# Kernel optimization log

Measured on AMD Instinct MI355X. Metric: run time of the kernel, lower is better.

## Reference

```python
import jax, jax.numpy as jnp
import numpy as np

FOCAL = 525.0
CX, CY = 320.0, 240.0
W_PROJ = 0.33   # loss_dict / energy_weights['proj']
W_BONE = 0.5    # loss_dict / energy_weights['bone']
B = 1_000_000
J = 21          # NUM_OF_JOINTS for 'mpi' model
NB = J - 1      # number of bone connections


def setup_inputs() -> dict:
    key = jax.random.key(0)
    k1, k2, k3 = jax.random.split(key, 3)
    # Poses: random joints shifted +10 in z so they sit in front of the camera
    # (avoids perspective divide by ~0).
    pose = jax.random.normal(k1, (B, 3, J), dtype=jnp.float32)
    pose = pose.at[:, 2, :].add(10.0)
    projected_est = jax.random.normal(k2, (B, 2, J), dtype=jnp.float32)
    bone_lengths = jax.random.uniform(k3, (NB,), dtype=jnp.float32) + 0.1
    R_drone = jnp.eye(3, dtype=jnp.float32)            # drone orientation
    C_drone = jnp.zeros((3, 1), dtype=jnp.float32)     # drone position
    # kinematic chain over 21 joints -> 20 bones
    bone_connections = jnp.stack(
        [jnp.arange(NB, dtype=jnp.int64), jnp.arange(1, J, dtype=jnp.int64)], axis=1)
    return {
        "future_pose3d": pose,
        "projected_est": projected_est,
        "bone_lengths": bone_lengths,
        "R_drone": R_drone,
        "C_drone": C_drone,
        "bone_connections": bone_connections,
    }


def _project(pose, R, C):
    # take_bone_projection: 2D = K @ R^T (P - C), then perspective divide.
    # pose: [B,3,J]
    K = jnp.array([[FOCAL, 0.0, CX], [0.0, FOCAL, CY], [0.0, 0.0, 1.0]],
                  dtype=pose.dtype)
    M = K @ R.T                                   # [3,3]
    proj = jnp.einsum('kc,bcj->bkj', M, pose - C[None, :, :])  # [B,3,J]
    return proj[:, :2, :] / proj[:, 2:3, :]      # [B,2,J]


def reference(future_pose3d, projected_est, bone_lengths, R_drone, C_drone,
              bone_connections):
    # --- projection MSE (per-sample mse_loss, averaged over batch) ---
    p2d = _project(future_pose3d, R_drone, C_drone)           # [B,2,J]
    n_el = 2.0 * J
    proj_loss = jnp.mean(jnp.sum((p2d - projected_est) ** 2, axis=(1, 2)) / n_el)

    # --- bone-length loss: gathered squared bone lengths vs targets ---
    d = (future_pose3d[:, :, bone_connections[:, 0]]
         - future_pose3d[:, :, bone_connections[:, 1]])        # [B,3,NB]
    sq_len = jnp.sum(d ** 2, axis=1)                           # [B,NB]
    bone_loss = jnp.mean(jnp.sum((bone_lengths[None, :] - sq_len) ** 2, axis=1)
                         / (J - 1))

    return W_PROJ * proj_loss + W_BONE * bone_loss
```

## Files before the change

### kernel.cpp

```cpp
#include <hip/hip_runtime.h>


namespace {

constexpr float F_    = 525.0f;
constexpr float CX_   = 320.0f;
constexpr float CY_   = 240.0f;
constexpr float WPROJ = 0.33f / 42.0f;
constexpr float WBONE = 0.5f  / 20.0f;
constexpr int   NT    = 64;
constexpr int   TILE  = 64;
constexpr int   PF4   = TILE * 63 / 4;
constexpr int   EF4   = TILE * 42 / 4;
constexpr int   TF4   = PF4 + EF4;
constexpr int   RFULL = TF4 / NT;
constexpr int   REM   = TF4 - RFULL*NT;
constexpr int   DMA_N = RFULL + 1;
constexpr int   NBLK  = 768;

constexpr int wcnt(int vm, int lgkm) {
    return (vm & 0xF) | ((vm >> 4) << 14) | (0x7 << 4) | ((lgkm & 0xF) << 8);
}

__device__ __forceinline__ long lmin(long a, long b) { return a < b ? a : b; }

__global__ __launch_bounds__(NT)
void pose_loss_kernel(const float* __restrict__ pose,
                      const float* __restrict__ est,
                      const float* __restrict__ bl,
                      const float* __restrict__ Rm,
                      const float* __restrict__ Cd,
                      float* __restrict__ out,
                      int B)
{
    __shared__ float4 smem[2 * TF4];

    const int tid = threadIdx.x;
    const float4* pose4 = (const float4*)pose;
    const float4* est4  = (const float4*)est;
    const long pmax = (long)B * 63 / 4 - 1;
    const long emax = (long)B * 42 / 4 - 1;
    const int  ntiles = (B + TILE - 1) / TILE;

    const float r0 = Rm[0], r1 = Rm[1], r2 = Rm[2];
    const float r3 = Rm[3], r4 = Rm[4], r5 = Rm[5];
    const float r6 = Rm[6], r7 = Rm[7], r8 = Rm[8];
    const float m00 = F_ * r0 + CX_ * r2;
    const float m01 = F_ * r3 + CX_ * r5;
    const float m02 = F_ * r6 + CX_ * r8;
    const float m10 = F_ * r1 + CY_ * r2;
    const float m11 = F_ * r4 + CY_ * r5;
    const float m12 = F_ * r7 + CY_ * r8;
    const float m20 = r2, m21 = r5, m22 = r8;
    const float c0 = Cd[0], c1 = Cd[1], c2 = Cd[2];
    float blv[20];
    #pragma unroll
    for (int i = 0; i < 20; ++i) blv[i] = bl[i];

    auto dma = [&](long T, int buf) {
        const long pb = T * PF4;
        const long eb = T * EF4 - PF4;
        float4* dst = &smem[buf * TF4];
        #pragma unroll
        for (int r = 0; r < RFULL; ++r) {
            const int f = r * NT + tid;
            const float4* g = (f < PF4) ? (pose4 + lmin(pb + f, pmax))
                                        : (est4  + lmin(eb + f, emax));
            __builtin_amdgcn_global_load_lds(
                (const __attribute__((address_space(1))) void*)g,
                (__attribute__((address_space(3))) void*)(dst + r * NT),
                16, 0, 0);
        }
        if (tid < REM) {
            const long gi = lmin(eb + RFULL * NT + tid, emax);
            __builtin_amdgcn_global_load_lds(
                (const __attribute__((address_space(1))) void*)(est4 + gi),
                (__attribute__((address_space(3))) void*)(&smem[buf*TF4 + RFULL*NT]),
                16, 0, 0);
        }
    };

    float accP = 0.0f, accB = 0.0f;
    long T = blockIdx.x;
    if (T < ntiles) dma(T, 0);

    int i = 0;
    while (T < ntiles) {
        const long Tn = T + NBLK;
        __asm__ __volatile__("" ::: "memory");
        __builtin_amdgcn_s_waitcnt(wcnt(63, 0));
        if (Tn < ntiles) {
            dma(Tn, (i + 1) & 1);
            __builtin_amdgcn_s_waitcnt(wcnt(DMA_N, 15));
        } else {
            __builtin_amdgcn_s_waitcnt(wcnt(0, 15));
        }
        __asm__ __volatile__("" ::: "memory");

        const float* sm = (const float*)&smem[(i & 1) * TF4];
        const float* ps = sm + tid * 63;
        const float* es = sm + TILE * 63 + tid * 42;
        const bool valid = (T * TILE + tid) < (long)B;
        float proj = 0.0f, bone = 0.0f;
        float pvx = 0.f, pvy = 0.f, pvz = 0.f;
        #pragma unroll
        for (int j = 0; j < 21; ++j) {
            const float x = ps[j]      - c0;
            const float y = ps[21 + j] - c1;
            const float z = ps[42 + j] - c2;
            const float q0 = fmaf(m00, x, fmaf(m01, y, m02 * z));
            const float q1 = fmaf(m10, x, fmaf(m11, y, m12 * z));
            const float q2 = fmaf(m20, x, fmaf(m21, y, m22 * z));
            const float inv = __builtin_amdgcn_rcpf(q2);
            const float du = fmaf(q0, inv, -es[j]);
            const float dv = fmaf(q1, inv, -es[21 + j]);
            proj += du * du + dv * dv;
            if (j > 0) {
                const float dx = pvx - x, dy = pvy - y, dz = pvz - z;
                const float sq = dx * dx + dy * dy + dz * dz;
                const float e  = blv[j - 1] - sq;
                bone += e * e;
            }
            pvx = x; pvy = y; pvz = z;
        }
        accP += valid ? proj : 0.0f;
        accB += valid ? bone : 0.0f;

        T = Tn; ++i;
    }

    float acc = WPROJ * accP + WBONE * accB;
    #pragma unroll
    for (int off = 32; off > 0; off >>= 1)
        acc += __shfl_down(acc, off, 64);
    if (tid == 0)
        atomicAdd(out, acc * (1.0f / (float)B));
}

}

extern "C" void kernel_launch(void* const* d_in, const int* in_sizes, int n_in,
                              void* d_out, int out_size, void* d_ws, size_t ws_size,
                              hipStream_t stream) {
    const float* pose = (const float*)d_in[0];
    const float* est  = (const float*)d_in[1];
    const float* bl   = (const float*)d_in[2];
    const float* Rm   = (const float*)d_in[3];
    const float* Cd   = (const float*)d_in[4];
    float* out = (float*)d_out;

    const int B = in_sizes[0] / 63;

    hipMemsetAsync(out, 0, sizeof(float), stream);
    pose_loss_kernel<<<NBLK, NT, 0, stream>>>(pose, est, bl, Rm, Cd, out, B);
}
```

Before: 441.7 us.

## Split each sample's joints across four lanes with smaller tiles and more blocks

Shrinks the per-block tile from 64 to 16 samples and assigns four threads per sample, each handling a contiguous chunk of about five joints, so per-thread work per tile drops and many more blocks (2816) keep loads in flight. The camera offset is folded into a precomputed translation term, and bone targets are preloaded per lane. The cost is redundant neighbour-joint reads, more LDS bank traffic from the strided layout, and more atomics at the end.

Result: no change. 446.5 us (+1.1%).

```diff
diff --git a/kernel.cpp b/kernel.cpp
--- a/kernel.cpp
+++ b/kernel.cpp
@@ -9,14 +9,14 @@
 constexpr float WPROJ = 0.33f / 42.0f;
 constexpr float WBONE = 0.5f  / 20.0f;
 constexpr int   NT    = 64;
-constexpr int   TILE  = 64;
+constexpr int   TILE  = 16;
 constexpr int   PF4   = TILE * 63 / 4;
 constexpr int   EF4   = TILE * 42 / 4;
 constexpr int   TF4   = PF4 + EF4;
 constexpr int   RFULL = TF4 / NT;
 constexpr int   REM   = TF4 - RFULL*NT;
 constexpr int   DMA_N = RFULL + 1;
-constexpr int   NBLK  = 768;
+constexpr int   NBLK  = 2816;
 
 constexpr int wcnt(int vm, int lgkm) {
     return (vm & 0xF) | ((vm >> 4) << 14) | (0x7 << 4) | ((lgkm & 0xF) << 8);
@@ -33,14 +33,14 @@
                       float* __restrict__ out,
                       int B)
 {
-    __shared__ float4 smem[2 * TF4];
+    __shared__ float smf[2 * TF4 * 4];
 
     const int tid = threadIdx.x;
     const float4* pose4 = (const float4*)pose;
     const float4* est4  = (const float4*)est;
     const long pmax = (long)B * 63 / 4 - 1;
     const long emax = (long)B * 42 / 4 - 1;
-    const int  ntiles = (B + TILE - 1) / TILE;
+    const long ntiles = ((long)B + TILE - 1) / TILE;
 
     const float r0 = Rm[0], r1 = Rm[1], r2 = Rm[2];
     const float r3 = Rm[3], r4 = Rm[4], r5 = Rm[5];
@@ -53,14 +53,26 @@
     const float m12 = F_ * r7 + CY_ * r8;
     const float m20 = r2, m21 = r5, m22 = r8;
     const float c0 = Cd[0], c1 = Cd[1], c2 = Cd[2];
-    float blv[20];
+    const float t0 = m00 * c0 + m01 * c1 + m02 * c2;
+    const float t1 = m10 * c0 + m11 * c1 + m12 * c2;
+    const float t2 = m20 * c0 + m21 * c1 + m22 * c2;
+
+    const int  s_loc   = tid & 15;
+    const int  q       = tid >> 4;
+    const int  jstart  = (q == 0) ? 0 : (1 + 5 * q);
+    const int  cntq    = (q == 0) ? 6 : 5;
+    float blk[6];
     #pragma unroll
-    for (int i = 0; i < 20; ++i) blv[i] = bl[i];
+    for (int k = 0; k < 6; ++k) {
+        int bi = jstart + k - 1;
+        bi = bi < 0 ? 0 : (bi > 19 ? 19 : bi);
+        blk[k] = bl[bi];
+    }
 
     auto dma = [&](long T, int buf) {
         const long pb = T * PF4;
         const long eb = T * EF4 - PF4;
-        float4* dst = &smem[buf * TF4];
+        float4* dst = (float4*)&smf[buf * TF4 * 4];
         #pragma unroll
         for (int r = 0; r < RFULL; ++r) {
             const int f = r * NT + tid;
@@ -75,7 +87,7 @@
             const long gi = lmin(eb + RFULL * NT + tid, emax);
             __builtin_amdgcn_global_load_lds(
                 (const __attribute__((address_space(1))) void*)(est4 + gi),
-                (__attribute__((address_space(3))) void*)(&smem[buf*TF4 + RFULL*NT]),
+                (__attribute__((address_space(3))) void*)(dst + RFULL * NT),
                 16, 0, 0);
         }
     };
@@ -86,7 +98,7 @@
 
     int i = 0;
     while (T < ntiles) {
-        const long Tn = T + NBLK;
+        const long Tn = T + gridDim.x;
         __asm__ __volatile__("" ::: "memory");
         __builtin_amdgcn_s_waitcnt(wcnt(63, 0));
         if (Tn < ntiles) {
@@ -97,34 +109,36 @@
         }
         __asm__ __volatile__("" ::: "memory");
 
-        const float* sm = (const float*)&smem[(i & 1) * TF4];
-        const float* ps = sm + tid * 63;
-        const float* es = sm + TILE * 63 + tid * 42;
-        const bool valid = (T * TILE + tid) < (long)B;
-        float proj = 0.0f, bone = 0.0f;
-        float pvx = 0.f, pvy = 0.f, pvz = 0.f;
+        const float* sm = &smf[(i & 1) * TF4 * 4];
+        const int pb = s_loc * 63;
+        const int eb = TILE * 63 + s_loc * 42;
+        const bool valid = (T * TILE + s_loc) < (long)B;
+
+        const int jp = (jstart > 0) ? jstart - 1 : 0;
+        float pvx = sm[pb + jp], pvy = sm[pb + 21 + jp], pvz = sm[pb + 42 + jp];
         #pragma unroll
-        for (int j = 0; j < 21; ++j) {
-            const float x = ps[j]      - c0;
-            const float y = ps[21 + j] - c1;
-            const float z = ps[42 + j] - c2;
-            const float q0 = fmaf(m00, x, fmaf(m01, y, m02 * z));
-            const float q1 = fmaf(m10, x, fmaf(m11, y, m12 * z));
-            const float q2 = fmaf(m20, x, fmaf(m21, y, m22 * z));
+        for (int k = 0; k < 6; ++k) {
+            const int j = jstart + k;
+            const float x = sm[pb + j];
+            const float y = sm[pb + 21 + j];
+            const float z = sm[pb + 42 + j];
+            const float u = sm[eb + j];
+            const float v = sm[eb + 21 + j];
+            const float q0 = fmaf(m00, x, fmaf(m01, y, fmaf(m02, z, -t0)));
+            const float q1 = fmaf(m10, x, fmaf(m11, y, fmaf(m12, z, -t1)));
+            const float q2 = fmaf(m20, x, fmaf(m21, y, fmaf(m22, z, -t2)));
             const float inv = __builtin_amdgcn_rcpf(q2);
-            const float du = fmaf(q0, inv, -es[j]);
-            const float dv = fmaf(q1, inv, -es[21 + j]);
-            proj += du * du + dv * dv;
-            if (j > 0) {
-                const float dx = pvx - x, dy = pvy - y, dz = pvz - z;
-                const float sq = dx * dx + dy * dy + dz * dz;
-                const float e  = blv[j - 1] - sq;
-                bone += e * e;
-            }
+            const float du = fmaf(q0, inv, -u);
+            const float dv = fmaf(q1, inv, -v);
+            const float pt = du * du + dv * dv;
+            const bool act = valid && (k < cntq);
+            accP += act ? pt : 0.0f;
+            const float dx = pvx - x, dy = pvy - y, dz = pvz - z;
+            const float sq = dx * dx + dy * dy + dz * dz;
+            const float e  = blk[k] - sq;
+            accB += (act && j > 0) ? e * e : 0.0f;
             pvx = x; pvy = y; pvz = z;
         }
-        accP += valid ? proj : 0.0f;
-        accB += valid ? bone : 0.0f;
 
         T = Tn; ++i;
     }
@@ -152,5 +166,7 @@
     const int B = in_sizes[0] / 63;
 
     hipMemsetAsync(out, 0, sizeof(float), stream);
-    pose_loss_kernel<<<NBLK, NT, 0, stream>>>(pose, est, bl, Rm, Cd, out, B);
+    const long ntiles = ((long)B + TILE - 1) / TILE;
+    const int  grid   = (int)(ntiles < NBLK ? ntiles : NBLK);
+    pose_loss_kernel<<<grid, NT, 0, stream>>>(pose, est, bl, Rm, Cd, out, B);
 }
```
